# Kernel optimization log

Measured on AMD Instinct MI355X. Metric: run time of the kernel, lower is better.

The kernel has to match this reference:

```python
import jax, jax.numpy as jnp
import numpy as np

EMBED_DIM = 1024
NUM_HEADS = 16
HEAD_DIM = EMBED_DIM // NUM_HEADS
WINDOW = 64


def apply_rope(x):
    # x: (B, H, S, d), rotate-half RoPE with base 10000
    B, H, S, d = x.shape
    half = d // 2
    pos = jnp.arange(S, dtype=x.dtype)
    freqs = 1.0 / (10000.0 ** (jnp.arange(half, dtype=x.dtype) / half))
    ang = pos[:, None] * freqs[None, :]              # (S, half)
    cos, sin = jnp.cos(ang), jnp.sin(ang)
    x1, x2 = x[..., :half], x[..., half:]
    return jnp.concatenate([x1 * cos - x2 * sin, x1 * sin + x2 * cos], axis=-1)


def setup_inputs() -> dict:
    key = jax.random.key(0)
    ks = jax.random.split(key, 12)
    B, S, D = 1, 2048, EMBED_DIM
    scale = 1.0 / np.sqrt(D)
    inp = {
        'query': jax.random.normal(ks[0], (B, S, D), jnp.float32),
        'key':   jax.random.normal(ks[1], (B, S, D), jnp.float32),
        'value': jax.random.normal(ks[2], (B, S, D), jnp.float32),
        'q_w': jax.random.normal(ks[3], (D, D), jnp.float32) * scale,
        'q_b': jax.random.normal(ks[4], (D,), jnp.float32) * 0.01,
        'k_w': jax.random.normal(ks[5], (D, D), jnp.float32) * scale,
        'k_b': jax.random.normal(ks[6], (D,), jnp.float32) * 0.01,
        'v_w': jax.random.normal(ks[7], (D, D), jnp.float32) * scale,
        'v_b': jax.random.normal(ks[8], (D,), jnp.float32) * 0.01,
        'o_w': jax.random.normal(ks[9], (D, D), jnp.float32) * scale,
        'o_b': jax.random.normal(ks[10], (D,), jnp.float32) * 0.01,
    }
    return inp


def _forward(query, key, value, q_w, q_b, k_w, k_b, v_w, v_b, o_w, o_b):
    B, S_q, D = query.shape
    S_k = key.shape[1]
    H, d, W = NUM_HEADS, HEAD_DIM, WINDOW

    q = (query @ q_w.T + q_b).reshape(B, S_q, H, d).transpose(0, 2, 1, 3)
    k = (key   @ k_w.T + k_b).reshape(B, S_k, H, d).transpose(0, 2, 1, 3)
    v = (value @ v_w.T + v_b).reshape(B, S_k, H, d).transpose(0, 2, 1, 3)

    q = apply_rope(q) * (d ** -0.5)
    k = apply_rope(k)

    # window indices: for query i, kv positions i-W .. i (invalid -> masked)
    q_pos = jnp.arange(S_q)[:, None]
    offsets = jnp.arange(-W, 1)[None, :]
    idx = q_pos + offsets                       # (S_q, W+1)
    local_mask = (idx < 0) | (idx >= S_k)       # (S_q, W+1)
    gidx = jnp.clip(idx, 0, S_k - 1)

    k_win = k[:, :, gidx, :]                    # (B, H, S_q, W+1, d)
    v_win = v[:, :, gidx, :]

    scores = jnp.einsum('bhqd,bhqwd->bhqw', q, k_win)
    mask = local_mask[None, None, :, :]
    scores = jnp.where(mask, -jnp.inf, scores)

    # safe softmax: fully-masked rows produce zeros
    m = jnp.max(scores, axis=-1, keepdims=True)
    m = jnp.where(jnp.isfinite(m), m, 0.0)
    e = jnp.exp(scores - m)
    denom = jnp.sum(e, axis=-1, keepdims=True)
    probs = jnp.where(denom > 0, e / jnp.where(denom > 0, denom, 1.0), 0.0)

    ctx = jnp.einsum('bhqw,bhqwd->bhqd', probs, v_win)
    ctx = ctx.transpose(0, 2, 1, 3).reshape(B, S_q, D)
    return ctx @ o_w.T + o_b


def reference(query, key, value, q_w, q_b, k_w, k_b, v_w, v_b, o_w, o_b):
    return _forward(query, key, value, q_w, q_b, k_w, k_b, v_w, v_b, o_w, o_b)
```

## Files before the change

### kernel.cpp

```cpp
#include <hip/hip_runtime.h>
#include <hip/hip_bf16.h>
#include <cstdint>
#include <cstddef>

typedef __attribute__((ext_vector_type(8))) short short8;
typedef __attribute__((ext_vector_type(4))) float f32x4;

__device__ __forceinline__ unsigned short f2bf(float f) {
  union { float f; uint32_t u; } c; c.f = f;
  uint32_t u = c.u;
  u += 0x7fffu + ((u >> 16) & 1u);
  return (unsigned short)(u >> 16);
}

__device__ __forceinline__ void gload16(const void* g, void* l) {
  __builtin_amdgcn_global_load_lds(
      (const __attribute__((address_space(1))) uint32_t*)g,
      (__attribute__((address_space(3))) uint32_t*)l, 16, 0, 0);
}

__global__ __launch_bounds__(256) void cvt_all(
    const float* __restrict__ q, const float* __restrict__ k, const float* __restrict__ v,
    const float* __restrict__ qw, const float* __restrict__ kw,
    const float* __restrict__ vw, const float* __restrict__ ow,
    unsigned short* __restrict__ qb, unsigned short* __restrict__ kb,
    unsigned short* __restrict__ vb, unsigned short* __restrict__ wqb,
    unsigned short* __restrict__ wkb, unsigned short* __restrict__ wvb,
    unsigned short* __restrict__ wob) {
  int i = blockIdx.x * 256 + threadIdx.x;
  const float* src; unsigned short* dst; int off;
  if (i < 1572864) {
    int seg = i >> 19; off = i & 524287;
    src = seg == 0 ? q : seg == 1 ? k : v;
    dst = seg == 0 ? qb : seg == 1 ? kb : vb;
  } else {
    int t = i - 1572864;
    int seg = t >> 18; off = t & 262143;
    src = seg == 0 ? qw : seg == 1 ? kw : seg == 2 ? vw : ow;
    dst = seg == 0 ? wqb : seg == 1 ? wkb : seg == 2 ? wvb : wob;
  }
  float4 x = reinterpret_cast<const float4*>(src)[off];
  ushort4 o;
  o.x = f2bf(x.x); o.y = f2bf(x.y); o.z = f2bf(x.z); o.w = f2bf(x.w);
  reinterpret_cast<ushort4*>(dst)[off] = o;
}

__global__ __launch_bounds__(512) void qkv_gemm(
    const unsigned short* __restrict__ Aq, const unsigned short* __restrict__ Ak,
    const unsigned short* __restrict__ Av,
    const unsigned short* __restrict__ Wq, const unsigned short* __restrict__ Wk,
    const unsigned short* __restrict__ Wv,
    const float* __restrict__ bq, const float* __restrict__ bk,
    const float* __restrict__ bv,
    unsigned short* __restrict__ Oq, unsigned short* __restrict__ Ok,
    unsigned short* __restrict__ OvT) {
  __shared__ __align__(16) unsigned short As[2][128][32];
  __shared__ __align__(16) unsigned short Bs[2][128][32];
  const int tid = threadIdx.x;
  const int w = tid >> 6, l = tid & 63;
  const int which = blockIdx.x >> 3;
  const int n0 = (blockIdx.x & 7) * 128;
  const int m0 = blockIdx.y * 128;
  const unsigned short* A = which == 0 ? Aq : which == 1 ? Ak : Av;
  const unsigned short* W = which == 0 ? Wq : which == 1 ? Wk : Wv;

  f32x4 acc[2][4];
#pragma unroll
  for (int a = 0; a < 2; ++a)
#pragma unroll
    for (int b = 0; b < 4; ++b) acc[a][b] = (f32x4){0.f, 0.f, 0.f, 0.f};

  const int wm = w >> 1, wn = w & 1;
  const int lr = l & 15, kq = l >> 4;
  const int srow = tid >> 2;
  const int scol = (tid & 3) * 8;

  auto stage = [&](int b, int kt) {
    const int k0 = kt * 32;
    gload16(A + (size_t)(m0 + srow) * 1024 + k0 + scol, (char*)&As[b][0][0] + tid * 16);
    gload16(W + (size_t)(n0 + srow) * 1024 + k0 + scol, (char*)&Bs[b][0][0] + tid * 16);
  };

  stage(0, 0);
  __syncthreads();

#pragma unroll 2
  for (int kt = 0; kt < 32; ++kt) {
    const int cur = kt & 1;
    if (kt < 31) stage(cur ^ 1, kt + 1);
    short8 af[2], bf[4];
#pragma unroll
    for (int f = 0; f < 2; ++f)
      af[f] = *reinterpret_cast<const short8*>(&As[cur][wm * 32 + f * 16 + lr][kq * 8]);
#pragma unroll
    for (int f = 0; f < 4; ++f)
      bf[f] = *reinterpret_cast<const short8*>(&Bs[cur][wn * 64 + f * 16 + lr][kq * 8]);
#pragma unroll
    for (int fm = 0; fm < 2; ++fm)
#pragma unroll
      for (int fn = 0; fn < 4; ++fn)
        acc[fm][fn] = __builtin_amdgcn_mfma_f32_16x16x32_bf16(af[fm], bf[fn], acc[fm][fn], 0, 0, 0);
    __syncthreads();
  }

  const float* bias = which == 0 ? bq : which == 1 ? bk : bv;
  if (which < 2) {
    unsigned short* Out = which == 0 ? Oq : Ok;
    const float sc = which == 0 ? 0.125f : 1.0f;
#pragma unroll
    for (int fn = 0; fn < 2; ++fn) {
      const int c1 = n0 + wn * 64 + fn * 16 + lr;
      const int c2 = c1 + 32;
      const int t = fn * 16 + lr;
      const float freq = exp2f(-(float)t * 0.415241012f);
      const float b1 = bias[c1], b2 = bias[c2];
#pragma unroll
      for (int fm = 0; fm < 2; ++fm) {
        const int rbase = m0 + wm * 32 + fm * 16 + kq * 4;
#pragma unroll
        for (int j = 0; j < 4; ++j) {
          const int s = rbase + j;
          float sn, cs;
          __sincosf((float)s * freq, &sn, &cs);
          const float x1 = acc[fm][fn][j] + b1;
          const float x2 = acc[fm][fn + 2][j] + b2;
          Out[(size_t)s * 1024 + c1] = f2bf((x1 * cs - x2 * sn) * sc);
          Out[(size_t)s * 1024 + c2] = f2bf((x1 * sn + x2 * cs) * sc);
        }
      }
    }
  } else {
#pragma unroll
    for (int fn = 0; fn < 4; ++fn) {
      const int c = n0 + wn * 64 + fn * 16 + lr;
      const float bb = bias[c];
#pragma unroll
      for (int fm = 0; fm < 2; ++fm) {
        const int rbase = m0 + wm * 32 + fm * 16 + kq * 4;
        ushort4 o;
        o.x = f2bf(acc[fm][fn][0] + bb);
        o.y = f2bf(acc[fm][fn][1] + bb);
        o.z = f2bf(acc[fm][fn][2] + bb);
        o.w = f2bf(acc[fm][fn][3] + bb);
        *reinterpret_cast<ushort4*>(OvT + (size_t)c * 2048 + rbase) = o;
      }
    }
  }
}

__global__ __launch_bounds__(256) void attn_kernel(
    const unsigned short* __restrict__ qr, const unsigned short* __restrict__ kr,
    const unsigned short* __restrict__ vT, unsigned short* __restrict__ ctx) {
  __shared__ __align__(16) unsigned short Ps[4][16][128];
  const int w = threadIdx.x >> 6, l = threadIdx.x & 63;
  const int h = blockIdx.x & 15, qb = blockIdx.x >> 4;
  const int i0 = qb * 64, hb = h * 64;
  const int r = l & 15, g = l >> 4;

  short8 qf[2];
#pragma unroll
  for (int kk = 0; kk < 2; ++kk)
    qf[kk] = *reinterpret_cast<const short8*>(
        qr + (size_t)(i0 + w * 16 + r) * 1024 + hb + kk * 32 + g * 8);

  f32x4 acc[8];
#pragma unroll
  for (int nt = 0; nt < 8; ++nt) acc[nt] = (f32x4){0.f, 0.f, 0.f, 0.f};
#pragma unroll
  for (int nt = 0; nt < 8; ++nt) {
    int kpos = i0 - 64 + nt * 16 + r;
    int krow = kpos < 0 ? 0 : kpos;
    const unsigned short* kp = kr + (size_t)krow * 1024 + hb + g * 8;
    short8 kf0 = *reinterpret_cast<const short8*>(kp);
    short8 kf1 = *reinterpret_cast<const short8*>(kp + 32);
    acc[nt] = __builtin_amdgcn_mfma_f32_16x16x32_bf16(qf[0], kf0, acc[nt], 0, 0, 0);
    acc[nt] = __builtin_amdgcn_mfma_f32_16x16x32_bf16(qf[1], kf1, acc[nt], 0, 0, 0);
  }

#pragma unroll
  for (int j = 0; j < 4; ++j) {
    const int iq = w * 16 + g * 4 + j;
    float sv[8];
    float m = -1e30f;
#pragma unroll
    for (int nt = 0; nt < 8; ++nt) {
      const int rel = nt * 16 + r - iq;
      const int kpos = i0 - 64 + nt * 16 + r;
      const bool ok = (rel >= 0) && (rel <= 64) && (kpos >= 0);
      sv[nt] = ok ? acc[nt][j] : -1e30f;
      m = fmaxf(m, sv[nt]);
    }
#pragma unroll
    for (int off = 8; off; off >>= 1) m = fmaxf(m, __shfl_xor(m, off));
    float e[8], den = 0.f;
#pragma unroll
    for (int nt = 0; nt < 8; ++nt) { e[nt] = __expf(sv[nt] - m); den += e[nt]; }
#pragma unroll
    for (int off = 8; off; off >>= 1) den += __shfl_xor(den, off);
    const float inv = 1.f / den;
    const int qrow = g * 4 + j;
    const int sw = (qrow & 7) << 3;
#pragma unroll
    for (int nt = 0; nt < 8; ++nt)
      Ps[w][qrow][(nt * 16 + r) ^ sw] = f2bf(e[nt] * inv);
  }

  __syncthreads();

  short8 pf[4];
  const int swr = (r & 7) << 3;
#pragma unroll
  for (int kk = 0; kk < 4; ++kk)
    pf[kk] = *reinterpret_cast<const short8*>(&Ps[w][r][(kk * 32 + g * 8) ^ swr]);

  f32x4 co[4];
#pragma unroll
  for (int n = 0; n < 4; ++n) co[n] = (f32x4){0.f, 0.f, 0.f, 0.f};
#pragma unroll
  for (int kk = 0; kk < 4; ++kk) {
    int cb = i0 - 64 + kk * 32 + g * 8;
    if (cb < 0) cb = 0;
#pragma unroll
    for (int n = 0; n < 4; ++n) {
      short8 vf = *reinterpret_cast<const short8*>(
          vT + (size_t)(hb + n * 16 + r) * 2048 + cb);
      co[n] = __builtin_amdgcn_mfma_f32_16x16x32_bf16(pf[kk], vf, co[n], 0, 0, 0);
    }
  }

#pragma unroll
  for (int n = 0; n < 4; ++n)
#pragma unroll
    for (int j = 0; j < 4; ++j)
      ctx[(size_t)(i0 + w * 16 + g * 4 + j) * 1024 + hb + n * 16 + r] = f2bf(co[n][j]);
}

__global__ __launch_bounds__(512) void oproj_gemm(
    const unsigned short* __restrict__ A, const unsigned short* __restrict__ W,
    const float* __restrict__ bias, float* __restrict__ Out) {
  __shared__ __align__(16) unsigned short As[2][128][32];
  __shared__ __align__(16) unsigned short Bs[2][64][32];
  const int tid = threadIdx.x;
  const int w = tid >> 6, l = tid & 63;
  const int n0 = blockIdx.x * 64;
  const int m0 = blockIdx.y * 128;

  f32x4 acc[2][2];
#pragma unroll
  for (int a = 0; a < 2; ++a)
#pragma unroll
    for (int b = 0; b < 2; ++b) acc[a][b] = (f32x4){0.f, 0.f, 0.f, 0.f};

  const int wm = w >> 1, wn = w & 1;
  const int lr = l & 15, kq = l >> 4;
  const int srow = tid >> 2;
  const int scol = (tid & 3) * 8;

  auto stage = [&](int b, int kt) {
    const int k0 = kt * 32;
    gload16(A + (size_t)(m0 + srow) * 1024 + k0 + scol, (char*)&As[b][0][0] + tid * 16);
    if (tid < 256)
      gload16(W + (size_t)(n0 + srow) * 1024 + k0 + scol, (char*)&Bs[b][0][0] + tid * 16);
  };

  stage(0, 0);
  __syncthreads();

#pragma unroll 2
  for (int kt = 0; kt < 32; ++kt) {
    const int cur = kt & 1;
    if (kt < 31) stage(cur ^ 1, kt + 1);
    short8 af[2], bf[2];
#pragma unroll
    for (int f = 0; f < 2; ++f)
      af[f] = *reinterpret_cast<const short8*>(&As[cur][wm * 32 + f * 16 + lr][kq * 8]);
#pragma unroll
    for (int f = 0; f < 2; ++f)
      bf[f] = *reinterpret_cast<const short8*>(&Bs[cur][wn * 32 + f * 16 + lr][kq * 8]);
#pragma unroll
    for (int fm = 0; fm < 2; ++fm)
#pragma unroll
      for (int fn = 0; fn < 2; ++fn)
        acc[fm][fn] = __builtin_amdgcn_mfma_f32_16x16x32_bf16(af[fm], bf[fn], acc[fm][fn], 0, 0, 0);
    __syncthreads();
  }

#pragma unroll
  for (int fm = 0; fm < 2; ++fm) {
    const int rbase = m0 + wm * 32 + fm * 16 + kq * 4;
#pragma unroll
    for (int fn = 0; fn < 2; ++fn) {
      const int c = n0 + wn * 32 + fn * 16 + lr;
      const float bb = bias[c];
#pragma unroll
      for (int j = 0; j < 4; ++j)
        Out[(size_t)(rbase + j) * 1024 + c] = acc[fm][fn][j] + bb;
    }
  }
}

extern "C" void kernel_launch(void* const* d_in, const int* in_sizes, int n_in,
                              void* d_out, int out_size, void* d_ws, size_t ws_size,
                              hipStream_t stream) {
  const float* query = (const float*)d_in[0];
  const float* key   = (const float*)d_in[1];
  const float* value = (const float*)d_in[2];
  const float* q_w = (const float*)d_in[3];
  const float* q_b = (const float*)d_in[4];
  const float* k_w = (const float*)d_in[5];
  const float* k_b = (const float*)d_in[6];
  const float* v_w = (const float*)d_in[7];
  const float* v_b = (const float*)d_in[8];
  const float* o_w = (const float*)d_in[9];
  const float* o_b = (const float*)d_in[10];
  float* out = (float*)d_out;

  unsigned short* ws = (unsigned short*)d_ws;
  unsigned short* qbf = ws;
  unsigned short* kbf = qbf + 2097152;
  unsigned short* vbf = kbf + 2097152;
  unsigned short* wqb = vbf + 2097152;
  unsigned short* wkb = wqb + 1048576;
  unsigned short* wvb = wkb + 1048576;
  unsigned short* wob = wvb + 1048576;
  unsigned short* qrope = wob + 1048576;
  unsigned short* krope = qrope + 2097152;
  unsigned short* vTb   = krope + 2097152;
  unsigned short* ctxb  = vTb + 2097152;

  cvt_all<<<10240, 256, 0, stream>>>(query, key, value, q_w, k_w, v_w, o_w,
                                     qbf, kbf, vbf, wqb, wkb, wvb, wob);
  qkv_gemm<<<dim3(24, 16), 512, 0, stream>>>(qbf, kbf, vbf, wqb, wkb, wvb,
                                             q_b, k_b, v_b, qrope, krope, vTb);
  attn_kernel<<<512, 256, 0, stream>>>(qrope, krope, vTb, ctxb);
  oproj_gemm<<<dim3(16, 16), 512, 0, stream>>>(ctxb, wob, o_b, out);
}
```

Before: 74.14 us.

## Fuse fp32-to-bf16 conversion into GEMM tile loads and drop convert kernel

Removes the separate cvt_all pass that converted inputs and weights to bf16 in workspace. The QKV and output-projection GEMMs now load fp32 tiles into registers, convert and pack them to bf16, and write them to LDS after the MFMAs of the current step, giving register-staged double buffering. This saves one kernel launch and a full read-plus-write round trip of about 28 MB. In exchange each GEMM block reads twice the bytes per tile, repeats the conversion across blocks that share a tile, and gives up the asynchronous direct global-to-LDS loads.

```diff
diff --git a/kernel.cpp b/kernel.cpp
--- a/kernel.cpp
+++ b/kernel.cpp
@@ -13,43 +13,21 @@
   return (unsigned short)(u >> 16);
 }
 
+__device__ __forceinline__ uint32_t pk_bf2(float lo, float hi) {
+  return (uint32_t)f2bf(lo) | ((uint32_t)f2bf(hi) << 16);
+}
+
 __device__ __forceinline__ void gload16(const void* g, void* l) {
   __builtin_amdgcn_global_load_lds(
       (const __attribute__((address_space(1))) uint32_t*)g,
       (__attribute__((address_space(3))) uint32_t*)l, 16, 0, 0);
 }
 
-__global__ __launch_bounds__(256) void cvt_all(
-    const float* __restrict__ q, const float* __restrict__ k, const float* __restrict__ v,
-    const float* __restrict__ qw, const float* __restrict__ kw,
-    const float* __restrict__ vw, const float* __restrict__ ow,
-    unsigned short* __restrict__ qb, unsigned short* __restrict__ kb,
-    unsigned short* __restrict__ vb, unsigned short* __restrict__ wqb,
-    unsigned short* __restrict__ wkb, unsigned short* __restrict__ wvb,
-    unsigned short* __restrict__ wob) {
-  int i = blockIdx.x * 256 + threadIdx.x;
-  const float* src; unsigned short* dst; int off;
-  if (i < 1572864) {
-    int seg = i >> 19; off = i & 524287;
-    src = seg == 0 ? q : seg == 1 ? k : v;
-    dst = seg == 0 ? qb : seg == 1 ? kb : vb;
-  } else {
-    int t = i - 1572864;
-    int seg = t >> 18; off = t & 262143;
-    src = seg == 0 ? qw : seg == 1 ? kw : seg == 2 ? vw : ow;
-    dst = seg == 0 ? wqb : seg == 1 ? wkb : seg == 2 ? wvb : wob;
-  }
-  float4 x = reinterpret_cast<const float4*>(src)[off];
-  ushort4 o;
-  o.x = f2bf(x.x); o.y = f2bf(x.y); o.z = f2bf(x.z); o.w = f2bf(x.w);
-  reinterpret_cast<ushort4*>(dst)[off] = o;
-}
-
 __global__ __launch_bounds__(512) void qkv_gemm(
-    const unsigned short* __restrict__ Aq, const unsigned short* __restrict__ Ak,
-    const unsigned short* __restrict__ Av,
-    const unsigned short* __restrict__ Wq, const unsigned short* __restrict__ Wk,
-    const unsigned short* __restrict__ Wv,
+    const float* __restrict__ Aq, const float* __restrict__ Ak,
+    const float* __restrict__ Av,
+    const float* __restrict__ Wq, const float* __restrict__ Wk,
+    const float* __restrict__ Wv,
     const float* __restrict__ bq, const float* __restrict__ bk,
     const float* __restrict__ bv,
     unsigned short* __restrict__ Oq, unsigned short* __restrict__ Ok,
@@ -61,8 +39,8 @@
   const int which = blockIdx.x >> 3;
   const int n0 = (blockIdx.x & 7) * 128;
   const int m0 = blockIdx.y * 128;
-  const unsigned short* A = which == 0 ? Aq : which == 1 ? Ak : Av;
-  const unsigned short* W = which == 0 ? Wq : which == 1 ? Wk : Wv;
+  const float* A = which == 0 ? Aq : which == 1 ? Ak : Av;
+  const float* W = which == 0 ? Wq : which == 1 ? Wk : Wv;
 
   f32x4 acc[2][4];
 #pragma unroll
@@ -75,19 +53,31 @@
   const int srow = tid >> 2;
   const int scol = (tid & 3) * 8;
 
-  auto stage = [&](int b, int kt) {
-    const int k0 = kt * 32;
-    gload16(A + (size_t)(m0 + srow) * 1024 + k0 + scol, (char*)&As[b][0][0] + tid * 16);
-    gload16(W + (size_t)(n0 + srow) * 1024 + k0 + scol, (char*)&Bs[b][0][0] + tid * 16);
-  };
-
-  stage(0, 0);
+  float4 ra0, ra1, rw0, rw1;
+  auto gload = [&](int kt) {
+    const float* pa = A + (size_t)(m0 + srow) * 1024 + kt * 32 + scol;
+    ra0 = *reinterpret_cast<const float4*>(pa);
+    ra1 = *reinterpret_cast<const float4*>(pa + 4);
+    const float* pw = W + (size_t)(n0 + srow) * 1024 + kt * 32 + scol;
+    rw0 = *reinterpret_cast<const float4*>(pw);
+    rw1 = *reinterpret_cast<const float4*>(pw + 4);
+  };
+  auto lwrite = [&](int b) {
+    uint4 va = make_uint4(pk_bf2(ra0.x, ra0.y), pk_bf2(ra0.z, ra0.w),
+                          pk_bf2(ra1.x, ra1.y), pk_bf2(ra1.z, ra1.w));
+    uint4 vw = make_uint4(pk_bf2(rw0.x, rw0.y), pk_bf2(rw0.z, rw0.w),
+                          pk_bf2(rw1.x, rw1.y), pk_bf2(rw1.z, rw1.w));
+    *reinterpret_cast<uint4*>(&As[b][srow][scol]) = va;
+    *reinterpret_cast<uint4*>(&Bs[b][srow][scol]) = vw;
+  };
+
+  gload(0);
+  lwrite(0);
   __syncthreads();
 
-#pragma unroll 2
   for (int kt = 0; kt < 32; ++kt) {
     const int cur = kt & 1;
-    if (kt < 31) stage(cur ^ 1, kt + 1);
+    if (kt < 31) gload(kt + 1);
     short8 af[2], bf[4];
 #pragma unroll
     for (int f = 0; f < 2; ++f)
@@ -100,6 +90,7 @@
 #pragma unroll
       for (int fn = 0; fn < 4; ++fn)
         acc[fm][fn] = __builtin_amdgcn_mfma_f32_16x16x32_bf16(af[fm], bf[fn], acc[fm][fn], 0, 0, 0);
+    if (kt < 31) lwrite(cur ^ 1);
     __syncthreads();
   }
 
@@ -236,7 +227,7 @@
 }
 
 __global__ __launch_bounds__(512) void oproj_gemm(
-    const unsigned short* __restrict__ A, const unsigned short* __restrict__ W,
+    const unsigned short* __restrict__ A, const float* __restrict__ W,
     const float* __restrict__ bias, float* __restrict__ Out) {
   __shared__ __align__(16) unsigned short As[2][128][32];
   __shared__ __align__(16) unsigned short Bs[2][64][32];
@@ -255,21 +246,30 @@
   const int lr = l & 15, kq = l >> 4;
   const int srow = tid >> 2;
   const int scol = (tid & 3) * 8;
-
-  auto stage = [&](int b, int kt) {
-    const int k0 = kt * 32;
-    gload16(A + (size_t)(m0 + srow) * 1024 + k0 + scol, (char*)&As[b][0][0] + tid * 16);
-    if (tid < 256)
-      gload16(W + (size_t)(n0 + srow) * 1024 + k0 + scol, (char*)&Bs[b][0][0] + tid * 16);
-  };
-
-  stage(0, 0);
+  const int wrow = tid >> 3;
+  const int wcol = (tid & 7) * 4;
+
+  float4 rw;
+  auto stageA = [&](int b, int kt) {
+    gload16(A + (size_t)(m0 + srow) * 1024 + kt * 32 + scol,
+            (char*)&As[b][0][0] + tid * 16);
+  };
+  auto gloadW = [&](int kt) {
+    rw = *reinterpret_cast<const float4*>(W + (size_t)(n0 + wrow) * 1024 + kt * 32 + wcol);
+  };
+  auto lwriteW = [&](int b) {
+    uint2 vw = make_uint2(pk_bf2(rw.x, rw.y), pk_bf2(rw.z, rw.w));
+    *reinterpret_cast<uint2*>(&Bs[b][wrow][wcol]) = vw;
+  };
+
+  stageA(0, 0);
+  gloadW(0);
+  lwriteW(0);
   __syncthreads();
 
-#pragma unroll 2
   for (int kt = 0; kt < 32; ++kt) {
     const int cur = kt & 1;
-    if (kt < 31) stage(cur ^ 1, kt + 1);
+    if (kt < 31) { stageA(cur ^ 1, kt + 1); gloadW(kt + 1); }
     short8 af[2], bf[2];
 #pragma unroll
     for (int f = 0; f < 2; ++f)
@@ -282,6 +282,7 @@
 #pragma unroll
       for (int fn = 0; fn < 2; ++fn)
         acc[fm][fn] = __builtin_amdgcn_mfma_f32_16x16x32_bf16(af[fm], bf[fn], acc[fm][fn], 0, 0, 0);
+    if (kt < 31) lwriteW(cur ^ 1);
     __syncthreads();
   }
 
@@ -316,22 +317,13 @@
   float* out = (float*)d_out;
 
   unsigned short* ws = (unsigned short*)d_ws;
-  unsigned short* qbf = ws;
-  unsigned short* kbf = qbf + 2097152;
-  unsigned short* vbf = kbf + 2097152;
-  unsigned short* wqb = vbf + 2097152;
-  unsigned short* wkb = wqb + 1048576;
-  unsigned short* wvb = wkb + 1048576;
-  unsigned short* wob = wvb + 1048576;
-  unsigned short* qrope = wob + 1048576;
+  unsigned short* qrope = ws;
   unsigned short* krope = qrope + 2097152;
   unsigned short* vTb   = krope + 2097152;
   unsigned short* ctxb  = vTb + 2097152;
 
-  cvt_all<<<10240, 256, 0, stream>>>(query, key, value, q_w, k_w, v_w, o_w,
-                                     qbf, kbf, vbf, wqb, wkb, wvb, wob);
-  qkv_gemm<<<dim3(24, 16), 512, 0, stream>>>(qbf, kbf, vbf, wqb, wkb, wvb,
+  qkv_gemm<<<dim3(24, 16), 512, 0, stream>>>(query, key, value, q_w, k_w, v_w,
                                              q_b, k_b, v_b, qrope, krope, vTb);
   attn_kernel<<<512, 256, 0, stream>>>(qrope, krope, vTb, ctxb);
-  oproj_gemm<<<dim3(16, 16), 512, 0, stream>>>(ctxb, wob, o_b, out);
-}
+  oproj_gemm<<<dim3(16, 16), 512, 0, stream>>>(ctxb, o_w, o_b, out);
+}
```

New measurement: 78.35 us. 1.06x slower.

## XOR-swizzle LDS tiles, deepen K tile in QKV GEMM, remap block order

Applied to the files above, without the earlier changes.

The QKV projection GEMM now stages 64-wide K tiles, doing 16 iterations instead of 32. Both it and the output-projection GEMM store LDS tiles with an XOR swizzle, applied on the global-side source offset and undone on the read, so fragment reads avoid bank conflicts. Block indices are also remapped (grouped by flat&7) to change which tiles run concurrently, likely for L2/XCD locality. The QKV kernel doubles its LDS footprint, which may reduce occupancy, and unroll pragmas were dropped.

```diff
diff --git a/kernel.cpp b/kernel.cpp
--- a/kernel.cpp
+++ b/kernel.cpp
@@ -45,6 +45,17 @@
   reinterpret_cast<ushort4*>(dst)[off] = o;
 }
 
+__device__ __forceinline__ short8 ldswz64(const unsigned short* base, int row, int sl) {
+  const int s = sl ^ (row & 7);
+  return *reinterpret_cast<const short8*>(
+      (const char*)base + row * 128 + s * 16);
+}
+__device__ __forceinline__ short8 ldswz32(const unsigned short* base, int row, int sl) {
+  const int s = sl ^ ((row >> 1) & 3);
+  return *reinterpret_cast<const short8*>(
+      (const char*)base + row * 64 + s * 16);
+}
+
 __global__ __launch_bounds__(512) void qkv_gemm(
     const unsigned short* __restrict__ Aq, const unsigned short* __restrict__ Ak,
     const unsigned short* __restrict__ Av,
@@ -54,13 +65,18 @@
     const float* __restrict__ bv,
     unsigned short* __restrict__ Oq, unsigned short* __restrict__ Ok,
     unsigned short* __restrict__ OvT) {
-  __shared__ __align__(16) unsigned short As[2][128][32];
-  __shared__ __align__(16) unsigned short Bs[2][128][32];
+  __shared__ __align__(16) unsigned short As[2][128][64];
+  __shared__ __align__(16) unsigned short Bs[2][128][64];
   const int tid = threadIdx.x;
   const int w = tid >> 6, l = tid & 63;
-  const int which = blockIdx.x >> 3;
-  const int n0 = (blockIdx.x & 7) * 128;
-  const int m0 = blockIdx.y * 128;
+
+  const int flat = blockIdx.y * 24 + blockIdx.x;
+  const int swz = (flat & 7) * 48 + (flat >> 3);
+  const int which = swz >> 7;
+  const int rem = swz & 127;
+  const int m0 = (rem >> 3) * 128;
+  const int n0 = (rem & 7) * 128;
+
   const unsigned short* A = which == 0 ? Aq : which == 1 ? Ak : Av;
   const unsigned short* W = which == 0 ? Wq : which == 1 ? Wk : Wv;
 
@@ -72,34 +88,46 @@
 
   const int wm = w >> 1, wn = w & 1;
   const int lr = l & 15, kq = l >> 4;
-  const int srow = tid >> 2;
-  const int scol = (tid & 3) * 8;
+
+  const int srow = tid >> 3;
+  const int ss = (tid & 7) ^ (srow & 7);
+  const unsigned short* pa0 = A + (size_t)(m0 + srow) * 1024 + ss * 8;
+  const unsigned short* pa1 = A + (size_t)(m0 + 64 + srow) * 1024 + ss * 8;
+  const unsigned short* pw0 = W + (size_t)(n0 + srow) * 1024 + ss * 8;
+  const unsigned short* pw1 = W + (size_t)(n0 + 64 + srow) * 1024 + ss * 8;
 
   auto stage = [&](int b, int kt) {
-    const int k0 = kt * 32;
-    gload16(A + (size_t)(m0 + srow) * 1024 + k0 + scol, (char*)&As[b][0][0] + tid * 16);
-    gload16(W + (size_t)(n0 + srow) * 1024 + k0 + scol, (char*)&Bs[b][0][0] + tid * 16);
+    const int k0 = kt * 64;
+    gload16(pa0 + k0, (char*)&As[b][0][0] + tid * 16);
+    gload16(pa1 + k0, (char*)&As[b][0][0] + 8192 + tid * 16);
+    gload16(pw0 + k0, (char*)&Bs[b][0][0] + tid * 16);
+    gload16(pw1 + k0, (char*)&Bs[b][0][0] + 8192 + tid * 16);
   };
 
   stage(0, 0);
   __syncthreads();
 
-#pragma unroll 2
-  for (int kt = 0; kt < 32; ++kt) {
+  for (int kt = 0; kt < 16; ++kt) {
     const int cur = kt & 1;
-    if (kt < 31) stage(cur ^ 1, kt + 1);
-    short8 af[2], bf[4];
-#pragma unroll
-    for (int f = 0; f < 2; ++f)
-      af[f] = *reinterpret_cast<const short8*>(&As[cur][wm * 32 + f * 16 + lr][kq * 8]);
-#pragma unroll
-    for (int f = 0; f < 4; ++f)
-      bf[f] = *reinterpret_cast<const short8*>(&Bs[cur][wn * 64 + f * 16 + lr][kq * 8]);
-#pragma unroll
-    for (int fm = 0; fm < 2; ++fm)
-#pragma unroll
-      for (int fn = 0; fn < 4; ++fn)
-        acc[fm][fn] = __builtin_amdgcn_mfma_f32_16x16x32_bf16(af[fm], bf[fn], acc[fm][fn], 0, 0, 0);
+    if (kt < 15) stage(cur ^ 1, kt + 1);
+    short8 af[2][2], bf[4][2];
+#pragma unroll
+    for (int kk = 0; kk < 2; ++kk) {
+#pragma unroll
+      for (int f = 0; f < 2; ++f)
+        af[f][kk] = ldswz64(&As[cur][0][0], wm * 32 + f * 16 + lr, kk * 4 + kq);
+#pragma unroll
+      for (int f = 0; f < 4; ++f)
+        bf[f][kk] = ldswz64(&Bs[cur][0][0], wn * 64 + f * 16 + lr, kk * 4 + kq);
+    }
+#pragma unroll
+    for (int kk = 0; kk < 2; ++kk)
+#pragma unroll
+      for (int fm = 0; fm < 2; ++fm)
+#pragma unroll
+        for (int fn = 0; fn < 4; ++fn)
+          acc[fm][fn] = __builtin_amdgcn_mfma_f32_16x16x32_bf16(
+              af[fm][kk], bf[fn][kk], acc[fm][fn], 0, 0, 0);
     __syncthreads();
   }
 
@@ -242,8 +270,11 @@
   __shared__ __align__(16) unsigned short Bs[2][64][32];
   const int tid = threadIdx.x;
   const int w = tid >> 6, l = tid & 63;
-  const int n0 = blockIdx.x * 64;
-  const int m0 = blockIdx.y * 128;
+
+  const int flat = blockIdx.y * 16 + blockIdx.x;
+  const int swz = (flat & 7) * 32 + (flat >> 3);
+  const int n0 = (swz & 15) * 64;
+  const int m0 = (swz >> 4) * 128;
 
   f32x4 acc[2][2];
 #pragma unroll
@@ -253,30 +284,32 @@
 
   const int wm = w >> 1, wn = w & 1;
   const int lr = l & 15, kq = l >> 4;
+
   const int srow = tid >> 2;
-  const int scol = (tid & 3) * 8;
+  const int ss = (tid & 3) ^ ((srow >> 1) & 3);
+  const unsigned short* pa = A + (size_t)(m0 + srow) * 1024 + ss * 8;
+  const unsigned short* pw = W + (size_t)(n0 + srow) * 1024 + ss * 8;
 
   auto stage = [&](int b, int kt) {
     const int k0 = kt * 32;
-    gload16(A + (size_t)(m0 + srow) * 1024 + k0 + scol, (char*)&As[b][0][0] + tid * 16);
+    gload16(pa + k0, (char*)&As[b][0][0] + tid * 16);
     if (tid < 256)
-      gload16(W + (size_t)(n0 + srow) * 1024 + k0 + scol, (char*)&Bs[b][0][0] + tid * 16);
+      gload16(pw + k0, (char*)&Bs[b][0][0] + tid * 16);
   };
 
   stage(0, 0);
   __syncthreads();
 
-#pragma unroll 2
   for (int kt = 0; kt < 32; ++kt) {
     const int cur = kt & 1;
     if (kt < 31) stage(cur ^ 1, kt + 1);
     short8 af[2], bf[2];
 #pragma unroll
     for (int f = 0; f < 2; ++f)
-      af[f] = *reinterpret_cast<const short8*>(&As[cur][wm * 32 + f * 16 + lr][kq * 8]);
+      af[f] = ldswz32(&As[cur][0][0], wm * 32 + f * 16 + lr, kq);
 #pragma unroll
     for (int f = 0; f < 2; ++f)
-      bf[f] = *reinterpret_cast<const short8*>(&Bs[cur][wn * 32 + f * 16 + lr][kq * 8]);
+      bf[f] = ldswz32(&Bs[cur][0][0], wn * 32 + f * 16 + lr, kq);
 #pragma unroll
     for (int fm = 0; fm < 2; ++fm)
 #pragma unroll
```

Result: faster. 64.07 us (-13.6%).
